# Kernel tuning notes

Hardware: AMD Instinct MI355X
Metric: run time of the kernel (lower is better)

Reference implementation:

```python
import jax, jax.numpy as jnp
import numpy as np

DT, TAU = 0.02, 0.1


def setup_inputs() -> dict:
    key = jax.random.key(0)
    ks = jax.random.split(key, 7)
    B, T, IN, H = 64, 2048, 64, 256
    return {
        "x0": jax.random.normal(ks[0], (B, H), jnp.float32),
        "I": jax.random.normal(ks[1], (B, T, IN), jnp.float32),
        "W_in": jax.random.normal(ks[2], (H, IN), jnp.float32) / np.sqrt(IN),
        "W_rec": jax.random.normal(ks[3], (H, H), jnp.float32) / np.sqrt(H),
        "b": jax.random.normal(ks[4], (H,), jnp.float32) * 0.1,
        "Wout": jax.random.normal(ks[5], (2, H), jnp.float32) / np.sqrt(H),
        "bout": jax.random.normal(ks[6], (2,), jnp.float32) * 0.1,
    }


def reference(x0, I, W_in, W_rec, b, Wout, bout):
    # Continuous-time leaky RNN, forward-Euler integration.
    # u_{t+1} = (1 - dt/tau) * u_t + (dt/tau) * (tanh(u_t) @ W_rec^T + I_t @ W_in^T + b)
    alpha = DT / TAU

    def step(u, I_t):
        r = jnp.tanh(u)                                   # [B, H]
        drive = r @ W_rec.T + I_t @ W_in.T + b            # [B, H]
        u_new = (1.0 - alpha) * u + alpha * drive
        return u_new, u_new

    I_tbf = jnp.swapaxes(I, 0, 1)                         # [T, B, IN]
    _, us = jax.lax.scan(step, x0, I_tbf)                 # [T, B, H]
    u = jnp.swapaxes(us, 0, 1)                            # [B, T, H]
    y = u @ Wout.T + bout                                 # [B, T, 2] linear readout
    return u, y
```

## Files before the change

kernel.cpp:

```cpp
#include <hip/hip_runtime.h>

#define BB 64
#define TT 2048
#define INW 64
#define HH 256

typedef float v2f __attribute__((ext_vector_type(2)));

__device__ __forceinline__ v2f fma2(v2f a, v2f b, v2f c) {
#if __has_builtin(__builtin_elementwise_fma)
    return __builtin_elementwise_fma(a, b, c);
#else
    v2f r; r.x = __builtin_fmaf(a.x, b.x, c.x); r.y = __builtin_fmaf(a.y, b.y, c.y); return r;
#endif
}

__device__ __forceinline__ float fast_tanh(float x) {
    float e = __expf(2.0f * x);
    return 1.0f - 2.0f / (e + 1.0f);
}

__device__ __forceinline__ void lds_barrier() {
    asm volatile("s_waitcnt lgkmcnt(0)" ::: "memory");
    __builtin_amdgcn_s_barrier();
    __builtin_amdgcn_sched_barrier(0);
}

__global__ __launch_bounds__(1024, 4)
void rnn_scan(const float* __restrict__ x0,
              const float* __restrict__ I,
              const float* __restrict__ W_in,
              const float* __restrict__ W_rec,
              const float* __restrict__ bias,
              float* __restrict__ u_out)
{
    __shared__ __align__(16) float r_buf[HH];
    __shared__ __align__(16) float i_buf[INW];
    __shared__ float part[8][HH + 8];

    const int b   = blockIdx.x;
    const int tid = threadIdx.x;
    const int h2  = tid & 127;
    const int q   = tid >> 7;
    const int k0  = q * 32;
    const int j0  = q * 8;
    const int hA  = h2;
    const int hB  = h2 + 128;
    const int il  = tid - 256;

    v2f wrA[16], wrB[16], wiA[4], wiB[4];
    {
        const float4* wa = (const float4*)(W_rec + (size_t)hA * HH + k0);
        const float4* wb = (const float4*)(W_rec + (size_t)hB * HH + k0);
        #pragma unroll
        for (int i = 0; i < 8; ++i) {
            float4 a = wa[i], bq = wb[i];
            wrA[2*i]     = (v2f){a.x, a.y};   wrA[2*i + 1] = (v2f){a.z, a.w};
            wrB[2*i]     = (v2f){bq.x, bq.y}; wrB[2*i + 1] = (v2f){bq.z, bq.w};
        }
        const float4* ia = (const float4*)(W_in + (size_t)hA * INW + j0);
        const float4* ib = (const float4*)(W_in + (size_t)hB * INW + j0);
        {
            float4 a = ia[0], bq = ib[0];
            wiA[0] = (v2f){a.x, a.y};   wiA[1] = (v2f){a.z, a.w};
            wiB[0] = (v2f){bq.x, bq.y}; wiB[1] = (v2f){bq.z, bq.w};
            a = ia[1]; bq = ib[1];
            wiA[2] = (v2f){a.x, a.y};   wiA[3] = (v2f){a.z, a.w};
            wiB[2] = (v2f){bq.x, bq.y}; wiB[3] = (v2f){bq.z, bq.w};
        }
    }

    float u = 0.0f, bv = 0.0f;
    if (tid < HH) {
        u  = x0[(size_t)b * HH + tid];
        bv = bias[tid];
        r_buf[tid] = fast_tanh(u);
    }
    if (tid < INW) i_buf[tid] = I[((size_t)b * TT + 0) * INW + tid];
    __syncthreads();

    const float4* rb4 = (const float4*)&r_buf[k0];
    const float4* ib4 = (const float4*)&i_buf[j0];

    for (int t = 0; t < TT; ++t) {
        float i_next = 0.0f;
        if ((unsigned)il < 64u && (t + 1) < TT)
            i_next = I[((size_t)b * TT + (t + 1)) * INW + il];

        v2f aA0 = {0.f,0.f}, aA1 = {0.f,0.f}, aB0 = {0.f,0.f}, aB1 = {0.f,0.f};
        #pragma unroll
        for (int i = 0; i < 8; ++i) {
            float4 r4 = rb4[i];
            v2f r01 = (v2f){r4.x, r4.y}, r23 = (v2f){r4.z, r4.w};
            aA0 = fma2(wrA[2*i],     r01, aA0);
            aA1 = fma2(wrA[2*i + 1], r23, aA1);
            aB0 = fma2(wrB[2*i],     r01, aB0);
            aB1 = fma2(wrB[2*i + 1], r23, aB1);
        }
        {
            float4 r4 = ib4[0];
            v2f r01 = (v2f){r4.x, r4.y}, r23 = (v2f){r4.z, r4.w};
            aA0 = fma2(wiA[0], r01, aA0);  aA1 = fma2(wiA[1], r23, aA1);
            aB0 = fma2(wiB[0], r01, aB0);  aB1 = fma2(wiB[1], r23, aB1);
            r4 = ib4[1];
            r01 = (v2f){r4.x, r4.y}; r23 = (v2f){r4.z, r4.w};
            aA0 = fma2(wiA[2], r01, aA0);  aA1 = fma2(wiA[3], r23, aA1);
            aB0 = fma2(wiB[2], r01, aB0);  aB1 = fma2(wiB[3], r23, aB1);
        }
        v2f sA = aA0 + aA1, sB = aB0 + aB1;
        part[q][hA] = sA.x + sA.y;
        part[q][hB] = sB.x + sB.y;
        lds_barrier();

        if (tid < HH) {
            float d = (((part[0][tid] + part[1][tid]) + (part[2][tid] + part[3][tid])) +
                       ((part[4][tid] + part[5][tid]) + (part[6][tid] + part[7][tid]))) + bv;
            u = 0.8f * u + 0.2f * d;
            u_out[((size_t)b * TT + t) * HH + tid] = u;
            r_buf[tid] = fast_tanh(u);
        }
        if ((unsigned)il < 64u && (t + 1) < TT)
            i_buf[il] = i_next;
        lds_barrier();
    }
}

__global__ __launch_bounds__(256)
void readout(const float* __restrict__ u,
             const float* __restrict__ Wout,
             const float* __restrict__ bout,
             float* __restrict__ y)
{
    const int wid  = threadIdx.x >> 6;
    const int lane = threadIdx.x & 63;
    const size_t row = (size_t)blockIdx.x * 4 + wid;

    float4 uv = ((const float4*)(u + row * HH))[lane];
    float4 w0 = ((const float4*)Wout)[lane];
    float4 w1 = ((const float4*)(Wout + HH))[lane];

    float acc0 = uv.x * w0.x + uv.y * w0.y + uv.z * w0.z + uv.w * w0.w;
    float acc1 = uv.x * w1.x + uv.y * w1.y + uv.z * w1.z + uv.w * w1.w;

    #pragma unroll
    for (int m = 32; m >= 1; m >>= 1) {
        acc0 += __shfl_xor(acc0, m, 64);
        acc1 += __shfl_xor(acc1, m, 64);
    }
    if (lane == 0) {
        y[row * 2 + 0] = acc0 + bout[0];
        y[row * 2 + 1] = acc1 + bout[1];
    }
}

extern "C" void kernel_launch(void* const* d_in, const int* in_sizes, int n_in,
                              void* d_out, int out_size, void* d_ws, size_t ws_size,
                              hipStream_t stream) {
    const float* x0    = (const float*)d_in[0];
    const float* I     = (const float*)d_in[1];
    const float* W_in  = (const float*)d_in[2];
    const float* W_rec = (const float*)d_in[3];
    const float* bias  = (const float*)d_in[4];
    const float* Wout  = (const float*)d_in[5];
    const float* bout  = (const float*)d_in[6];

    float* u_out = (float*)d_out;
    float* y_out = u_out + (size_t)BB * TT * HH;

    rnn_scan<<<BB, 1024, 0, stream>>>(x0, I, W_in, W_rec, bias, u_out);
    readout<<<(BB * TT) / 4, 256, 0, stream>>>(u_out, Wout, bout, y_out);
}
```

Baseline: 1.553 ms.

## Precompute input projection in a parallel kernel, reuse output buffer for drive

Moves the I_t @ W_in^T + b projection out of the sequential scan into a separate fully parallel kernel that writes the projected drive into the u output buffer. The scan then loads one precomputed value per step, prefetched two steps ahead and double-buffered in LDS, and overwrites it in place with u. This removes eight FMAs per thread and the W_in registers from the latency-bound per-step loop. In exchange it adds an extra pass that writes and rereads a large B×T×H array through global memory, and a 256-float load per step instead of 64.

```diff
diff --git a/kernel.cpp b/kernel.cpp
--- a/kernel.cpp
+++ b/kernel.cpp
@@ -4,6 +4,8 @@
 #define TT 2048
 #define INW 64
 #define HH 256
+#define NXB 512
+#define RPB ((BB * TT) / NXB)
 
 typedef float v2f __attribute__((ext_vector_type(2)));
 
@@ -26,16 +28,48 @@
     __builtin_amdgcn_sched_barrier(0);
 }
 
+__global__ __launch_bounds__(256)
+void xprep(const float* __restrict__ I,
+           const float* __restrict__ W_in,
+           const float* __restrict__ bias,
+           float* __restrict__ X)
+{
+    const int h = threadIdx.x;
+    const size_t row0 = (size_t)blockIdx.x * RPB;
+
+    v2f w[32];
+    {
+        const float4* wp = (const float4*)(W_in + (size_t)h * INW);
+        #pragma unroll
+        for (int i = 0; i < 16; ++i) {
+            float4 a = wp[i];
+            w[2*i]     = (v2f){a.x, a.y};
+            w[2*i + 1] = (v2f){a.z, a.w};
+        }
+    }
+    const float bv = bias[h];
+
+    for (int r = 0; r < RPB; ++r) {
+        const float4* ip = (const float4*)(I + (row0 + r) * INW);
+        v2f acc0 = {0.f, 0.f}, acc1 = {0.f, 0.f};
+        #pragma unroll
+        for (int i = 0; i < 16; ++i) {
+            float4 iv = ip[i];
+            acc0 = fma2(w[2*i],     (v2f){iv.x, iv.y}, acc0);
+            acc1 = fma2(w[2*i + 1], (v2f){iv.z, iv.w}, acc1);
+        }
+        v2f s = acc0 + acc1;
+        X[(row0 + r) * HH + h] = s.x + s.y + bv;
+    }
+}
+
 __global__ __launch_bounds__(1024, 4)
 void rnn_scan(const float* __restrict__ x0,
-              const float* __restrict__ I,
-              const float* __restrict__ W_in,
               const float* __restrict__ W_rec,
-              const float* __restrict__ bias,
-              float* __restrict__ u_out)
+              float* uX)
 {
     __shared__ __align__(16) float r_buf[HH];
-    __shared__ __align__(16) float i_buf[INW];
+    __shared__ __align__(16) float xbuf[2][HH];
     __shared__ float part[8][HH + 8];
 
     const int b   = blockIdx.x;
@@ -43,12 +77,11 @@
     const int h2  = tid & 127;
     const int q   = tid >> 7;
     const int k0  = q * 32;
-    const int j0  = q * 8;
     const int hA  = h2;
     const int hB  = h2 + 128;
     const int il  = tid - 256;
 
-    v2f wrA[16], wrB[16], wiA[4], wiB[4];
+    v2f wrA[16], wrB[16];
     {
         const float4* wa = (const float4*)(W_rec + (size_t)hA * HH + k0);
         const float4* wb = (const float4*)(W_rec + (size_t)hB * HH + k0);
@@ -58,34 +91,26 @@
             wrA[2*i]     = (v2f){a.x, a.y};   wrA[2*i + 1] = (v2f){a.z, a.w};
             wrB[2*i]     = (v2f){bq.x, bq.y}; wrB[2*i + 1] = (v2f){bq.z, bq.w};
         }
-        const float4* ia = (const float4*)(W_in + (size_t)hA * INW + j0);
-        const float4* ib = (const float4*)(W_in + (size_t)hB * INW + j0);
-        {
-            float4 a = ia[0], bq = ib[0];
-            wiA[0] = (v2f){a.x, a.y};   wiA[1] = (v2f){a.z, a.w};
-            wiB[0] = (v2f){bq.x, bq.y}; wiB[1] = (v2f){bq.z, bq.w};
-            a = ia[1]; bq = ib[1];
-            wiA[2] = (v2f){a.x, a.y};   wiA[3] = (v2f){a.z, a.w};
-            wiB[2] = (v2f){bq.x, bq.y}; wiB[3] = (v2f){bq.z, bq.w};
-        }
     }
 
-    float u = 0.0f, bv = 0.0f;
+    float u = 0.0f;
     if (tid < HH) {
-        u  = x0[(size_t)b * HH + tid];
-        bv = bias[tid];
+        u = x0[(size_t)b * HH + tid];
         r_buf[tid] = fast_tanh(u);
     }
-    if (tid < INW) i_buf[tid] = I[((size_t)b * TT + 0) * INW + tid];
+    if (tid < 64)
+        ((float4*)&xbuf[0][0])[tid] = ((const float4*)(uX + (size_t)b * TT * HH))[tid];
+    float4 x_next = {0.f, 0.f, 0.f, 0.f};
+    if ((unsigned)il < 64u)
+        x_next = ((const float4*)(uX + ((size_t)b * TT + 1) * HH))[il];
     __syncthreads();
 
     const float4* rb4 = (const float4*)&r_buf[k0];
-    const float4* ib4 = (const float4*)&i_buf[j0];
 
     for (int t = 0; t < TT; ++t) {
-        float i_next = 0.0f;
-        if ((unsigned)il < 64u && (t + 1) < TT)
-            i_next = I[((size_t)b * TT + (t + 1)) * INW + il];
+        float4 x_fut = {0.f, 0.f, 0.f, 0.f};
+        if ((unsigned)il < 64u && (t + 2) < TT)
+            x_fut = ((const float4*)(uX + ((size_t)b * TT + t + 2) * HH))[il];
 
         v2f aA0 = {0.f,0.f}, aA1 = {0.f,0.f}, aB0 = {0.f,0.f}, aB1 = {0.f,0.f};
         #pragma unroll
@@ -97,16 +122,6 @@
             aB0 = fma2(wrB[2*i],     r01, aB0);
             aB1 = fma2(wrB[2*i + 1], r23, aB1);
         }
-        {
-            float4 r4 = ib4[0];
-            v2f r01 = (v2f){r4.x, r4.y}, r23 = (v2f){r4.z, r4.w};
-            aA0 = fma2(wiA[0], r01, aA0);  aA1 = fma2(wiA[1], r23, aA1);
-            aB0 = fma2(wiB[0], r01, aB0);  aB1 = fma2(wiB[1], r23, aB1);
-            r4 = ib4[1];
-            r01 = (v2f){r4.x, r4.y}; r23 = (v2f){r4.z, r4.w};
-            aA0 = fma2(wiA[2], r01, aA0);  aA1 = fma2(wiA[3], r23, aA1);
-            aB0 = fma2(wiB[2], r01, aB0);  aB1 = fma2(wiB[3], r23, aB1);
-        }
         v2f sA = aA0 + aA1, sB = aB0 + aB1;
         part[q][hA] = sA.x + sA.y;
         part[q][hB] = sB.x + sB.y;
@@ -114,13 +129,15 @@
 
         if (tid < HH) {
             float d = (((part[0][tid] + part[1][tid]) + (part[2][tid] + part[3][tid])) +
-                       ((part[4][tid] + part[5][tid]) + (part[6][tid] + part[7][tid]))) + bv;
+                       ((part[4][tid] + part[5][tid]) + (part[6][tid] + part[7][tid])))
+                      + xbuf[t & 1][tid];
             u = 0.8f * u + 0.2f * d;
-            u_out[((size_t)b * TT + t) * HH + tid] = u;
+            uX[((size_t)b * TT + t) * HH + tid] = u;
             r_buf[tid] = fast_tanh(u);
         }
         if ((unsigned)il < 64u && (t + 1) < TT)
-            i_buf[il] = i_next;
+            *(float4*)&xbuf[(t + 1) & 1][4 * il] = x_next;
+        x_next = x_fut;
         lds_barrier();
     }
 }
@@ -167,6 +184,7 @@
     float* u_out = (float*)d_out;
     float* y_out = u_out + (size_t)BB * TT * HH;
 
-    rnn_scan<<<BB, 1024, 0, stream>>>(x0, I, W_in, W_rec, bias, u_out);
+    xprep<<<NXB, 256, 0, stream>>>(I, W_in, bias, u_out);
+    rnn_scan<<<BB, 1024, 0, stream>>>(x0, W_rec, u_out);
     readout<<<(BB * TT) / 4, 256, 0, stream>>>(u_out, Wout, bout, y_out);
 }
```

Result: slower. 1.683 ms (+8.4%).
